# Kernel optimization log

Measured on AMD Instinct MI355X. Metric: run time of the kernel, lower is better.

The kernel has to match this reference:

```python
import jax, jax.numpy as jnp
import numpy as np

SIDELEN = 128
PIXEL_SZ = 1.0
PI = float(np.pi)
CHUNK = 128  # atoms per scan step; keeps per-step intermediate ~170 MB


def setup_inputs() -> dict:
    key = jax.random.key(0)
    k1, k2, k3 = jax.random.split(key, 3)
    coords = jax.random.normal(k1, (4, 2048, 3), dtype=jnp.float32) * 10.0  # angstrom-ish spread
    # form factors must be positive (ff_b appears as 4*pi/ff_b); keep away from 0
    ff_a = jax.random.uniform(k2, (2048, 5), dtype=jnp.float32, minval=0.5, maxval=2.0)
    ff_b = jax.random.uniform(k3, (2048, 5), dtype=jnp.float32, minval=0.5, maxval=2.0)
    return {"coords": coords, "ff_a": ff_a, "ff_b": ff_b}


def _grid_2d():
    ax = jnp.arange(-(SIDELEN // 2), (SIDELEN - 1) // 2 + 1, dtype=jnp.float32)
    X, Y = jnp.meshgrid(ax, ax, indexing="ij")  # torch.meshgrid default is 'ij'
    return jnp.stack([Y, X], axis=-1).reshape(-1, 2) * PIXEL_SZ  # [P, 2]


def _potential(coords2d, ff_a, ff_b, grid):
    # coords2d: [B, A, 2]; ff_a, ff_b: [A, 5]; grid: [P, 2]
    B, A, _ = coords2d.shape
    P = grid.shape[0]
    invb = (4.0 * PI) / ff_b                      # [A, 5]
    coef = ff_a * invb                            # [A, 5]
    nc = A // CHUNK
    ac = coords2d.reshape(B, nc, CHUNK, 2).transpose(1, 0, 2, 3)  # [nc, B, C, 2]
    ib = invb.reshape(nc, CHUNK, 5)
    cc = coef.reshape(nc, CHUNK, 5)

    def step(acc, chunk):
        a, ibc, ccc = chunk
        diff = grid[None, None, :, :] - a[:, :, None, :]          # [B, C, P, 2]
        d2 = jnp.sum(diff * diff, axis=-1)                        # [B, C, P]
        # dist_sq = invb * ||dx||^2 per form factor; contrib = exp(-pi*dist_sq)*ff_a*invb
        e = jnp.exp(-PI * ib_bcast(ibc) * d2[:, :, None, :])      # [B, C, 5, P]
        acc = acc + jnp.einsum("bcfp,cf->bp", e, ccc)
        return acc, None

    def ib_bcast(ibc):
        return ibc[None, :, :, None]  # [1, C, 5, 1]

    acc0 = jnp.zeros((B, P), dtype=coords2d.dtype)
    pot, _ = jax.lax.scan(step, acc0, (ac, ib, cc))
    return pot  # [B, P]


def reference(coords, ff_a, ff_b):
    B = coords.shape[0]
    grid = _grid_2d()
    pot = _potential(coords[..., :2], ff_a, ff_b, grid)
    return pot.reshape(B, 1, SIDELEN, SIDELEN)
```

## Files before the change

### kernel.cpp

```cpp
#include <hip/hip_runtime.h>

#define SIDE 128
#define PI_F 3.14159265358979f
#define RMAX 1.4f

__global__ void __launch_bounds__(256) potential_stripe(
        const float* __restrict__ coords,
        const float* __restrict__ ff_a,
        const float* __restrict__ ff_b,
        float* __restrict__ out,
        int A) {
    const int s    = blockIdx.x;
    const int b    = blockIdx.y;
    const int row0 = s * 2;
    const int t    = threadIdx.x;

    __shared__ float img[2 * SIDE];
    __shared__ int   cnt;
    __shared__ int   list[2048];

    img[t] = 0.0f;
    if (t == 0) cnt = 0;
    __syncthreads();

    const float* cb = coords + (size_t)b * A * 3;

    const float ylo = (float)row0 - RMAX;
    const float yhi = (float)(row0 + 1) + RMAX;
    for (int a = t; a < A; a += 256) {
        float x  = cb[a * 3 + 0];
        float y  = cb[a * 3 + 1];
        float cx = x + 64.0f;
        float cy = y + 64.0f;
        if (cy >= ylo && cy <= yhi && cx >= -RMAX && cx <= 127.0f + RMAX) {
            list[atomicAdd(&cnt, 1)] = a;
        }
    }
    __syncthreads();

    const int n = cnt;
    for (int k = t; k < n; k += 256) {
        int a = list[k];
        float cx = cb[a * 3 + 0] + 64.0f;
        float cy = cb[a * 3 + 1] + 64.0f;
        #pragma unroll
        for (int f = 0; f < 5; ++f) {
            float fa = ff_a[a * 5 + f];
            float fb = ff_b[a * 5 + f];
            float invb = (4.0f * PI_F) / fb;
            float coef = fa * invb;
            float c    = PI_F * invb;
            float r = sqrtf((__logf(coef) + 32.0f) / c);

            int i0 = max(row0,     (int)ceilf(cy - r));
            int i1 = min(row0 + 1, (int)floorf(cy + r));
            int j0 = max(0,        (int)ceilf(cx - r));
            int j1 = min(SIDE - 1, (int)floorf(cx + r));

            for (int i = i0; i <= i1; ++i) {
                float dy  = (float)i - cy;
                float wyi = coef * __expf(-c * dy * dy);
                float* rowp = img + (i - row0) * SIDE;
                for (int j = j0; j <= j1; ++j) {
                    float dx = (float)j - cx;
                    atomicAdd(&rowp[j], wyi * __expf(-c * dx * dx));
                }
            }
        }
    }
    __syncthreads();

    float4* ov = (float4*)(out + ((size_t)b * SIDE + row0) * SIDE);
    if (t < (2 * SIDE) / 4)
        ov[t] = ((const float4*)img)[t];
}

extern "C" void kernel_launch(void* const* d_in, const int* in_sizes, int n_in,
                              void* d_out, int out_size, void* d_ws, size_t ws_size,
                              hipStream_t stream) {
    const float* coords = (const float*)d_in[0];
    const float* ffa    = (const float*)d_in[1];
    const float* ffb    = (const float*)d_in[2];
    float* out = (float*)d_out;

    int A = in_sizes[1] / 5;
    int B = in_sizes[0] / (A * 3);

    dim3 grid(SIDE / 2, B);
    potential_stripe<<<grid, 256, 0, stream>>>(coords, ffa, ffb, out, A);
}
```

Measured before the change: 66.99 us.

## Use wave-aggregated atomics for atom culling, cache coords in LDS, double block size

The culling pass now uses a wavefront ballot and popcount, so each wave issues one shared atomicAdd instead of one per kept atom. The kept atoms' x/y coordinates are stored in shared memory next to their indices, which avoids reloading them from global memory in the splat loop. Block size rises from 256 to 512, so the culling loop needs fewer iterations. The cost is more LDS per block and idle threads in the splat phase, since each stripe typically keeps only a few atoms.

```diff
diff --git a/kernel.cpp b/kernel.cpp
--- a/kernel.cpp
+++ b/kernel.cpp
@@ -3,8 +3,9 @@
 #define SIDE 128
 #define PI_F 3.14159265358979f
 #define RMAX 1.4f
+#define BLK 512
 
-__global__ void __launch_bounds__(256) potential_stripe(
+__global__ void __launch_bounds__(BLK) potential_stripe(
         const float* __restrict__ coords,
         const float* __restrict__ ff_a,
         const float* __restrict__ ff_b,
@@ -14,12 +15,14 @@
     const int b    = blockIdx.y;
     const int row0 = s * 2;
     const int t    = threadIdx.x;
+    const int lane = t & 63;
 
     __shared__ float img[2 * SIDE];
     __shared__ int   cnt;
-    __shared__ int   list[2048];
+    __shared__ float lx[2048], ly[2048];
+    __shared__ int   li[2048];
 
-    img[t] = 0.0f;
+    if (t < 2 * SIDE) img[t] = 0.0f;
     if (t == 0) cnt = 0;
     __syncthreads();
 
@@ -27,22 +30,34 @@
 
     const float ylo = (float)row0 - RMAX;
     const float yhi = (float)(row0 + 1) + RMAX;
-    for (int a = t; a < A; a += 256) {
-        float x  = cb[a * 3 + 0];
-        float y  = cb[a * 3 + 1];
-        float cx = x + 64.0f;
-        float cy = y + 64.0f;
-        if (cy >= ylo && cy <= yhi && cx >= -RMAX && cx <= 127.0f + RMAX) {
-            list[atomicAdd(&cnt, 1)] = a;
+    for (int a0 = 0; a0 < A; a0 += BLK) {
+        int a = a0 + t;
+        float cx = 0.f, cy = 0.f;
+        bool keep = false;
+        if (a < A) {
+            cx = cb[a * 3 + 0] + 64.0f;
+            cy = cb[a * 3 + 1] + 64.0f;
+            keep = (cy >= ylo) & (cy <= yhi) &
+                   (cx >= -RMAX) & (cx <= 127.0f + RMAX);
+        }
+        unsigned long long m = __ballot(keep);
+        int nw  = __popcll(m);
+        int pos = __popcll(m & ((1ull << lane) - 1ull));
+        int base = 0;
+        if (lane == 0 && nw) base = atomicAdd(&cnt, nw);
+        base = __shfl(base, 0);
+        if (keep) {
+            int k = base + pos;
+            lx[k] = cx; ly[k] = cy; li[k] = a;
         }
     }
     __syncthreads();
 
     const int n = cnt;
-    for (int k = t; k < n; k += 256) {
-        int a = list[k];
-        float cx = cb[a * 3 + 0] + 64.0f;
-        float cy = cb[a * 3 + 1] + 64.0f;
+    for (int k = t; k < n; k += BLK) {
+        float cx = lx[k];
+        float cy = ly[k];
+        int   a  = li[k];
         #pragma unroll
         for (int f = 0; f < 5; ++f) {
             float fa = ff_a[a * 5 + f];
@@ -70,9 +85,10 @@
     }
     __syncthreads();
 
-    float4* ov = (float4*)(out + ((size_t)b * SIDE + row0) * SIDE);
-    if (t < (2 * SIDE) / 4)
+    if (t < (2 * SIDE) / 4) {
+        float4* ov = (float4*)(out + ((size_t)b * SIDE + row0) * SIDE);
         ov[t] = ((const float4*)img)[t];
+    }
 }
 
 extern "C" void kernel_launch(void* const* d_in, const int* in_sizes, int n_in,
@@ -87,5 +103,5 @@
     int B = in_sizes[0] / (A * 3);
 
     dim3 grid(SIDE / 2, B);
-    potential_stripe<<<grid, 256, 0, stream>>>(coords, ffa, ffb, out, A);
+    potential_stripe<<<grid, BLK, 0, stream>>>(coords, ffa, ffb, out, A);
 }
```

Result: faster. 64.15 us, median of 2 (-4.2%).
